# Kernel optimization log

Measured on AMD Instinct MI355X. Metric: run time of the kernel, lower is better.

## Reference

```python
import jax, jax.numpy as jnp
import numpy as np

B = 256   # batch == nodes (required by the module's mask broadcasting)
N = 256
F = 128   # in_features
H = 4     # num_heads
D = 8     # out_features (per-head dim)
E_RAND = 8192


def setup_inputs() -> dict:
    key = jax.random.key(0)
    ks = jax.random.split(key, 10)
    x = jax.random.normal(ks[0], (B, N, F), jnp.float32)
    # random edges + self-loops so every adjacency row is non-empty
    e = jax.random.randint(ks[1], (2, E_RAND), 0, B)
    diag = jnp.stack([jnp.arange(B), jnp.arange(B)])
    edge_index = jnp.concatenate([e, diag], axis=1)  # [2, 8448]
    s_in = 1.0 / np.sqrt(F)
    s_hd = 1.0 / np.sqrt(H * D)
    Wq = jax.random.normal(ks[2], (F, H * D), jnp.float32) * s_in
    Wk = jax.random.normal(ks[3], (F, H * D), jnp.float32) * s_in
    Wv = jax.random.normal(ks[4], (F, H * D), jnp.float32) * s_in
    Wo = jax.random.normal(ks[5], (H * D, D), jnp.float32) * s_hd
    bq = jax.random.normal(ks[6], (H * D,), jnp.float32) * s_in
    bk = jax.random.normal(ks[7], (H * D,), jnp.float32) * s_in
    bv = jax.random.normal(ks[8], (H * D,), jnp.float32) * s_in
    bo = jax.random.normal(ks[9], (D,), jnp.float32) * s_hd
    return dict(x=x, edge_index=edge_index, Wq=Wq, bq=bq, Wk=Wk, bk=bk,
                Wv=Wv, bv=bv, Wo=Wo, bo=bo)


def reference(x, edge_index, Wq, bq, Wk, bk, Wv, bv, Wo, bo):
    Bn, Nn, _ = x.shape
    q = (x @ Wq + bq).reshape(Bn, Nn, H, D)
    k = (x @ Wk + bk).reshape(Bn, Nn, H, D)
    v = (x @ Wv + bv).reshape(Bn, Nn, H, D)
    # [B, H, N, N]
    scores = jnp.einsum('bqhd,bkhd->bhqk', q, k) / jnp.sqrt(jnp.float32(D))
    # dense adjacency from sparse edge list, as in the original
    adj = jnp.zeros((Bn, Bn), x.dtype).at[edge_index[0], edge_index[1]].set(1.0)
    # mask [B,B] broadcasts over trailing (q,k) dims since N == B
    scores = jnp.where(adj == 0, -jnp.inf, scores)
    attn = jax.nn.softmax(scores, axis=-1)
    out = jnp.einsum('bhqk,bkhd->bqhd', attn, v).reshape(Bn, Nn, H * D)
    return out @ Wo + bo
```

## Files before the change

kernel.cpp:

```cpp
#include <hip/hip_runtime.h>

typedef unsigned int u32;
typedef __fp16 h2v __attribute__((ext_vector_type(2)));
typedef __fp16 h4 __attribute__((ext_vector_type(4)));
typedef float f32x16 __attribute__((ext_vector_type(16)));

#define NB 256
#define NNODE 256
#define FF 128
#define DD 8
#define HDIM 32

__device__ __forceinline__ float dot2(h2v a, h2v b, float c) {
  return __builtin_amdgcn_fdot2(a, b, c, false);
}
__device__ __forceinline__ h2v bch2(u32 u) { return __builtin_bit_cast(h2v, u); }
__device__ __forceinline__ h4 bch4(uint2 u) { return __builtin_bit_cast(h4, u); }
__device__ __forceinline__ u32 bcu(h2v v) { return __builtin_bit_cast(u32, v); }
__device__ __forceinline__ f32x16 fzero() {
  f32x16 z;
  #pragma unroll
  for (int r = 0; r < 16; ++r) z[r] = 0.f;
  return z;
}
__device__ __forceinline__ f32x16 mfma8(h4 a, h4 b, f32x16 c) {
  return __builtin_amdgcn_mfma_f32_32x32x8f16(a, b, c, 0, 0, 0);
}

__global__ __launch_bounds__(256) void prep_w_kernel(
    const float* __restrict__ Wq, const float* __restrict__ bq,
    const float* __restrict__ Wk, const float* __restrict__ bk,
    const float* __restrict__ Wv, const float* __restrict__ bv,
    const float* __restrict__ Wo,
    u32* __restrict__ mask, u32* __restrict__ WtH, float* __restrict__ bias,
    u32* __restrict__ woT2)
{
  int g = blockIdx.x * 256 + threadIdx.x;
  if (g < 96 * 64) {
    int c = g >> 6, f = (g & 63) * 2;
    const float* W = (c < 32) ? Wq : ((c < 64) ? Wk : Wv);
    int cc = c & 31;
    WtH[g] = bcu(__builtin_amdgcn_cvt_pkrtz(W[f*HDIM + cc], W[(f+1)*HDIM + cc]));
  }
  if (g < NNODE * 8) mask[g] = 0u;
  if (g < 96) {
    const float* bb = (g < 32) ? bq : ((g < 64) ? bk : bv);
    bias[g] = bb[g & 31];
  }
  if (g < 128) {
    int d = g >> 4, p = g & 15;
    woT2[g] = bcu(__builtin_amdgcn_cvt_pkrtz(Wo[(2*p)*DD + d], Wo[(2*p+1)*DD + d]));
  }
}

__global__ __launch_bounds__(256) void prep_e_kernel(
    const int* __restrict__ eidx, int E, u32* __restrict__ mask)
{
  int e = blockIdx.x * 256 + threadIdx.x;
  if (e < E) {
    int r = eidx[e], c = eidx[E + e];
    atomicOr(&mask[r*8 + (c >> 5)], 1u << (c & 31));
  }
}

__global__ __launch_bounds__(256, 2) void fused_kernel(
    const float* __restrict__ x, const u32* __restrict__ WtH,
    const float* __restrict__ bias, const u32* __restrict__ mask,
    const u32* __restrict__ woT2, const float* __restrict__ bo,
    float* __restrict__ out)
{
  __shared__ u32 wLds[96 * 66];
  __shared__ __fp16 kS[NNODE * 36];
  __shared__ __fp16 vt32[32 * 260];
  __shared__ __fp16 oS[128 * 36];
  __shared__ u32 woS[128];
  __shared__ float boS[8];

  int t = threadIdx.x, lane = t & 63, w = t >> 6;
  int l31 = lane & 31, hi = lane >> 5;
  int b = blockIdx.x >> 1, half = blockIdx.x & 1;

  for (int g = t; g < 96 * 64; g += 256)
    wLds[(g >> 6) * 66 + (g & 63)] = WtH[g];
  if (t < 128) woS[t] = woT2[t];
  if (t < 8) boS[t] = bo[t];

  f32x16 aq, ak0, av0, ak1, av1;
  #pragma unroll
  for (int r = 0; r < 16; ++r) aq[r] = bias[(r & 3) + 8*(r >> 2) + 4*hi];
  {
    float bk_ = bias[32 + l31], bv_ = bias[64 + l31];
    #pragma unroll
    for (int r = 0; r < 16; ++r) { ak0[r]=bk_; av0[r]=bv_; ak1[r]=bk_; av1[r]=bv_; }
  }

  int node = half*128 + w*32 + l31;
  uint4 m0 = *(const uint4*)(mask + node * 8);
  uint4 m1 = *(const uint4*)(mask + node * 8 + 4);
  u32 mw8[8] = { m0.x, m0.y, m0.z, m0.w, m1.x, m1.y, m1.z, m1.w };
  #pragma unroll
  for (int i = 0; i < 8; ++i) mw8[i] = hi ? (mw8[i] >> 4) : mw8[i];

  __syncthreads();

  const float* xr0 = x + ((size_t)b * NNODE + w*32 + l31) * FF + 4 * hi;
  const float* xr1 = xr0 + (size_t)128 * FF;
  #pragma unroll
  for (int ks = 0; ks < 16; ++ks) {
    float4 xf0 = *(const float4*)(xr0 + ks * 8);
    float4 xf1 = *(const float4*)(xr1 + ks * 8);
    h2v a0 = __builtin_amdgcn_cvt_pkrtz(xf0.x, xf0.y);
    h2v b0 = __builtin_amdgcn_cvt_pkrtz(xf0.z, xf0.w);
    h4 f0 = __builtin_shufflevector(a0, b0, 0, 1, 2, 3);
    h2v a1 = __builtin_amdgcn_cvt_pkrtz(xf1.x, xf1.y);
    h2v b1 = __builtin_amdgcn_cvt_pkrtz(xf1.z, xf1.w);
    h4 f1 = __builtin_shufflevector(a1, b1, 0, 1, 2, 3);
    h4 wk = bch4(*(const uint2*)&wLds[(32 + l31)*66 + ks*4 + 2*hi]);
    h4 wv = bch4(*(const uint2*)&wLds[(64 + l31)*66 + ks*4 + 2*hi]);
    h4 wq = bch4(*(const uint2*)&wLds[l31*66 + ks*4 + 2*hi]);
    ak0 = mfma8(f0, wk, ak0);
    ak1 = mfma8(f1, wk, ak1);
    av0 = mfma8(f0, wv, av0);
    av1 = mfma8(f1, wv, av1);
    aq  = mfma8(wq, half ? f1 : f0, aq);
  }
  #pragma unroll
  for (int r = 0; r < 16; ++r) {
    int rc = (r & 3) + 8*(r >> 2) + 4*hi;
    int n0 = w*32 + rc, n1 = n0 + 128;
    kS[n0 * 36 + l31] = (__fp16)ak0[r];
    kS[n1 * 36 + l31] = (__fp16)ak1[r];
    vt32[l31 * 260 + n0] = (__fp16)av0[r];
    vt32[l31 * 260 + n1] = (__fp16)av1[r];
  }
  h4 Qf[4];
  #pragma unroll
  for (int h = 0; h < 4; ++h) {
    h2v qa = __builtin_amdgcn_cvt_pkrtz(aq[4*h],     aq[4*h + 1]);
    h2v qb = __builtin_amdgcn_cvt_pkrtz(aq[4*h + 2], aq[4*h + 3]);
    Qf[h] = __builtin_shufflevector(qa, qb, 0, 1, 2, 3);
  }
  __syncthreads();

  const float sc2 = 0.51006977f;
  const h2v one2 = bch2(0x3C003C00u);
  f32x16 accO[4] = { fzero(), fzero(), fzero(), fzero() };
  float lp[4] = { 0.f, 0.f, 0.f, 0.f };
  #pragma unroll
  for (int kt = 0; kt < 8; ++kt) {
    u32 mwh = mw8[kt];
    float mbv[16];
    #pragma unroll
    for (int r = 0; r < 16; ++r) {
      int bp = (r & 3) + 8*(r >> 2);
      mbv[r] = ((mwh >> bp) & 1u) ? -8.0f : -1e30f;
    }
    u32 pw[4][8];
    #pragma unroll
    for (int h = 0; h < 4; ++h) {
      h4 Kf = bch4(*(const uint2*)&kS[(kt*32 + l31)*36 + 8*h + 4*hi]);
      f32x16 T = mfma8(Kf, Qf[h], fzero());
      #pragma unroll
      for (int j = 0; j < 8; ++j) {
        float p0 = __builtin_amdgcn_exp2f(__builtin_fmaf(T[2*j],   sc2, mbv[2*j]));
        float p1 = __builtin_amdgcn_exp2f(__builtin_fmaf(T[2*j+1], sc2, mbv[2*j+1]));
        pw[h][j] = bcu(__builtin_amdgcn_cvt_pkrtz(p0, p1));
        lp[h] = dot2(bch2(pw[h][j]), one2, lp[h]);
      }
    }
    __builtin_amdgcn_s_setprio(1);
    #pragma unroll
    for (int kk = 0; kk < 4; ++kk) {
      h4 va = bch4(*(const uint2*)&vt32[l31*260 + kt*32 + kk*8 + 4*hi]);
      #pragma unroll
      for (int h = 0; h < 4; ++h)
        accO[h] = mfma8(va, bch4(make_uint2(pw[h][2*kk], pw[h][2*kk+1])), accO[h]);
    }
    __builtin_amdgcn_s_setprio(0);
  }
  #pragma unroll
  for (int h = 0; h < 4; ++h) {
    float lq = lp[h] + __shfl_xor(lp[h], 32);
    float inv = 1.0f / lq;
    h2v o0 = __builtin_amdgcn_cvt_pkrtz(accO[h][4*h]*inv,   accO[h][4*h+1]*inv);
    h2v o1 = __builtin_amdgcn_cvt_pkrtz(accO[h][4*h+2]*inv, accO[h][4*h+3]*inv);
    *(uint2*)&oS[(w*32 + l31)*36 + 8*h + 4*hi] = make_uint2(bcu(o0), bcu(o1));
  }
  __syncthreads();

  int pr = t >> 1, d4 = (t & 1) * 4;
  float r4[4] = { boS[d4], boS[d4+1], boS[d4+2], boS[d4+3] };
  #pragma unroll
  for (int p = 0; p < 16; ++p) {
    h2v o2 = bch2(*(const u32*)&oS[pr*36 + 2*p]);
    #pragma unroll
    for (int d = 0; d < 4; ++d)
      r4[d] = dot2(o2, bch2(woS[(d4 + d)*16 + p]), r4[d]);
  }
  float4 o = { r4[0], r4[1], r4[2], r4[3] };
  *(float4*)(out + ((size_t)b * NNODE + half*128 + pr) * DD + d4) = o;
}

extern "C" void kernel_launch(void* const* d_in, const int* in_sizes, int n_in,
                              void* d_out, int out_size, void* d_ws, size_t ws_size,
                              hipStream_t stream)
{
  const float* x  = (const float*)d_in[0];
  const int*   ei = (const int*)d_in[1];
  const float* Wq = (const float*)d_in[2];
  const float* bq = (const float*)d_in[3];
  const float* Wk = (const float*)d_in[4];
  const float* bk = (const float*)d_in[5];
  const float* Wv = (const float*)d_in[6];
  const float* bv = (const float*)d_in[7];
  const float* Wo = (const float*)d_in[8];
  const float* bo = (const float*)d_in[9];
  int E = in_sizes[1] / 2;

  char* ws = (char*)d_ws;
  u32*   mask = (u32*)(ws + 0);
  u32*   WtH  = (u32*)(ws + 8192);
  float* bias = (float*)(ws + 32768);
  u32*   woT2 = (u32*)(ws + 33280);

  prep_w_kernel<<<24, 256, 0, stream>>>(Wq, bq, Wk, bk, Wv, bv, Wo,
                                        mask, WtH, bias, woT2);
  prep_e_kernel<<<(E + 255) / 256, 256, 0, stream>>>(ei, E, mask);
  fused_kernel<<<NB * 2, 256, 0, stream>>>(x, WtH, bias, mask, woT2, bo,
                                           (float*)d_out);
}
```

Measured before the change: 41.75 us.

## Merge prep kernels and fuse output projection into register epilogue

```diff
diff --git a/kernel.cpp b/kernel.cpp
--- a/kernel.cpp
+++ b/kernel.cpp
@@ -27,11 +27,11 @@
   return __builtin_amdgcn_mfma_f32_32x32x8f16(a, b, c, 0, 0, 0);
 }
 
-__global__ __launch_bounds__(256) void prep_w_kernel(
+__global__ __launch_bounds__(256) void prep_kernel(
     const float* __restrict__ Wq, const float* __restrict__ bq,
     const float* __restrict__ Wk, const float* __restrict__ bk,
     const float* __restrict__ Wv, const float* __restrict__ bv,
-    const float* __restrict__ Wo,
+    const float* __restrict__ Wo, const int* __restrict__ eidx, int E,
     u32* __restrict__ mask, u32* __restrict__ WtH, float* __restrict__ bias,
     u32* __restrict__ woT2)
 {
@@ -42,7 +42,6 @@
     int cc = c & 31;
     WtH[g] = bcu(__builtin_amdgcn_cvt_pkrtz(W[f*HDIM + cc], W[(f+1)*HDIM + cc]));
   }
-  if (g < NNODE * 8) mask[g] = 0u;
   if (g < 96) {
     const float* bb = (g < 32) ? bq : ((g < 64) ? bk : bv);
     bias[g] = bb[g & 31];
@@ -51,14 +50,8 @@
     int d = g >> 4, p = g & 15;
     woT2[g] = bcu(__builtin_amdgcn_cvt_pkrtz(Wo[(2*p)*DD + d], Wo[(2*p+1)*DD + d]));
   }
-}
-
-__global__ __launch_bounds__(256) void prep_e_kernel(
-    const int* __restrict__ eidx, int E, u32* __restrict__ mask)
-{
-  int e = blockIdx.x * 256 + threadIdx.x;
-  if (e < E) {
-    int r = eidx[e], c = eidx[E + e];
+  if (g < E) {
+    int r = eidx[g], c = eidx[E + g];
     atomicOr(&mask[r*8 + (c >> 5)], 1u << (c & 31));
   }
 }
@@ -72,7 +65,6 @@
   __shared__ u32 wLds[96 * 66];
   __shared__ __fp16 kS[NNODE * 36];
   __shared__ __fp16 vt32[32 * 260];
-  __shared__ __fp16 oS[128 * 36];
   __shared__ u32 woS[128];
   __shared__ float boS[8];
 
@@ -178,27 +170,28 @@
     }
     __builtin_amdgcn_s_setprio(0);
   }
+
+  float pa[8];
+  #pragma unroll
+  for (int dd = 0; dd < 8; ++dd) pa[dd] = 0.f;
   #pragma unroll
   for (int h = 0; h < 4; ++h) {
     float lq = lp[h] + __shfl_xor(lp[h], 32);
     float inv = 1.0f / lq;
-    h2v o0 = __builtin_amdgcn_cvt_pkrtz(accO[h][4*h]*inv,   accO[h][4*h+1]*inv);
-    h2v o1 = __builtin_amdgcn_cvt_pkrtz(accO[h][4*h+2]*inv, accO[h][4*h+3]*inv);
-    *(uint2*)&oS[(w*32 + l31)*36 + 8*h + 4*hi] = make_uint2(bcu(o0), bcu(o1));
-  }
-  __syncthreads();
-
-  int pr = t >> 1, d4 = (t & 1) * 4;
-  float r4[4] = { boS[d4], boS[d4+1], boS[d4+2], boS[d4+3] };
-  #pragma unroll
-  for (int p = 0; p < 16; ++p) {
-    h2v o2 = bch2(*(const u32*)&oS[pr*36 + 2*p]);
-    #pragma unroll
-    for (int d = 0; d < 4; ++d)
-      r4[d] = dot2(o2, bch2(woS[(d4 + d)*16 + p]), r4[d]);
-  }
-  float4 o = { r4[0], r4[1], r4[2], r4[3] };
-  *(float4*)(out + ((size_t)b * NNODE + half*128 + pr) * DD + d4) = o;
+    h2v o01 = __builtin_amdgcn_cvt_pkrtz(accO[h][4*h]*inv,   accO[h][4*h+1]*inv);
+    h2v o23 = __builtin_amdgcn_cvt_pkrtz(accO[h][4*h+2]*inv, accO[h][4*h+3]*inv);
+    #pragma unroll
+    for (int dd = 0; dd < 8; ++dd) {
+      pa[dd] = dot2(o01, bch2(woS[dd*16 + 4*h + 2*hi]),     pa[dd]);
+      pa[dd] = dot2(o23, bch2(woS[dd*16 + 4*h + 2*hi + 1]), pa[dd]);
+    }
+  }
+  #pragma unroll
+  for (int dd = 0; dd < 8; ++dd)
+    pa[dd] += __shfl_xor(pa[dd], 32);
+  float4 o4 = { pa[4*hi]   + boS[4*hi],   pa[4*hi+1] + boS[4*hi+1],
+                pa[4*hi+2] + boS[4*hi+2], pa[4*hi+3] + boS[4*hi+3] };
+  *(float4*)(out + ((size_t)b * NNODE + node) * DD + 4*hi) = o4;
 }
 
 extern "C" void kernel_launch(void* const* d_in, const int* in_sizes, int n_in,
@@ -223,9 +216,10 @@
   float* bias = (float*)(ws + 32768);
   u32*   woT2 = (u32*)(ws + 33280);
 
-  prep_w_kernel<<<24, 256, 0, stream>>>(Wq, bq, Wk, bk, Wv, bv, Wo,
-                                        mask, WtH, bias, woT2);
-  prep_e_kernel<<<(E + 255) / 256, 256, 0, stream>>>(ei, E, mask);
+  hipMemsetAsync(mask, 0, NNODE * 8 * sizeof(u32), stream);
+  int prep_work = (96*64 > E) ? 96*64 : E;
+  prep_kernel<<<(prep_work + 255)/256, 256, 0, stream>>>(
+      Wq, bq, Wk, bk, Wv, bv, Wo, ei, E, mask, WtH, bias, woT2);
   fused_kernel<<<NB * 2, 256, 0, stream>>>(x, WtH, bias, mask, woT2, bo,
                                            (float*)d_out);
 }
```

Measured after the change: 42.95 us. 1.03x slower.

## Merge prep kernels and split attention loop into two head-pair passes

Applied to the files above, without the earlier changes.

```diff
diff --git a/kernel.cpp b/kernel.cpp
--- a/kernel.cpp
+++ b/kernel.cpp
@@ -27,11 +27,11 @@
   return __builtin_amdgcn_mfma_f32_32x32x8f16(a, b, c, 0, 0, 0);
 }
 
-__global__ __launch_bounds__(256) void prep_w_kernel(
+__global__ __launch_bounds__(256) void prep_kernel(
     const float* __restrict__ Wq, const float* __restrict__ bq,
     const float* __restrict__ Wk, const float* __restrict__ bk,
     const float* __restrict__ Wv, const float* __restrict__ bv,
-    const float* __restrict__ Wo,
+    const float* __restrict__ Wo, const int* __restrict__ eidx, int E,
     u32* __restrict__ mask, u32* __restrict__ WtH, float* __restrict__ bias,
     u32* __restrict__ woT2)
 {
@@ -42,7 +42,6 @@
     int cc = c & 31;
     WtH[g] = bcu(__builtin_amdgcn_cvt_pkrtz(W[f*HDIM + cc], W[(f+1)*HDIM + cc]));
   }
-  if (g < NNODE * 8) mask[g] = 0u;
   if (g < 96) {
     const float* bb = (g < 32) ? bq : ((g < 64) ? bk : bv);
     bias[g] = bb[g & 31];
@@ -51,14 +50,8 @@
     int d = g >> 4, p = g & 15;
     woT2[g] = bcu(__builtin_amdgcn_cvt_pkrtz(Wo[(2*p)*DD + d], Wo[(2*p+1)*DD + d]));
   }
-}
-
-__global__ __launch_bounds__(256) void prep_e_kernel(
-    const int* __restrict__ eidx, int E, u32* __restrict__ mask)
-{
-  int e = blockIdx.x * 256 + threadIdx.x;
-  if (e < E) {
-    int r = eidx[e], c = eidx[E + e];
+  if (g < E) {
+    int r = eidx[g], c = eidx[E + g];
     atomicOr(&mask[r*8 + (c >> 5)], 1u << (c & 31));
   }
 }
@@ -144,47 +137,61 @@
 
   const float sc2 = 0.51006977f;
   const h2v one2 = bch2(0x3C003C00u);
-  f32x16 accO[4] = { fzero(), fzero(), fzero(), fzero() };
-  float lp[4] = { 0.f, 0.f, 0.f, 0.f };
-  #pragma unroll
-  for (int kt = 0; kt < 8; ++kt) {
-    u32 mwh = mw8[kt];
-    float mbv[16];
+  #pragma unroll
+  for (int hp = 0; hp < 2; ++hp) {
+    int h0 = 2*hp, h1 = 2*hp + 1;
+    f32x16 accO0 = fzero(), accO1 = fzero();
+    float lp0 = 0.f, lp1 = 0.f;
     #pragma unroll
-    for (int r = 0; r < 16; ++r) {
-      int bp = (r & 3) + 8*(r >> 2);
-      mbv[r] = ((mwh >> bp) & 1u) ? -8.0f : -1e30f;
+    for (int kt = 0; kt < 8; ++kt) {
+      u32 mwh = mw8[kt];
+      float mbv[16];
+      #pragma unroll
+      for (int r = 0; r < 16; ++r) {
+        int bp = (r & 3) + 8*(r >> 2);
+        mbv[r] = ((mwh >> bp) & 1u) ? -8.0f : -1e30f;
+      }
+      u32 pw0[8], pw1[8];
+      {
+        h4 Kf = bch4(*(const uint2*)&kS[(kt*32 + l31)*36 + 8*h0 + 4*hi]);
+        f32x16 T = mfma8(Kf, Qf[h0], fzero());
+        #pragma unroll
+        for (int j = 0; j < 8; ++j) {
+          float p0 = __builtin_amdgcn_exp2f(__builtin_fmaf(T[2*j],   sc2, mbv[2*j]));
+          float p1 = __builtin_amdgcn_exp2f(__builtin_fmaf(T[2*j+1], sc2, mbv[2*j+1]));
+          pw0[j] = bcu(__builtin_amdgcn_cvt_pkrtz(p0, p1));
+          lp0 = dot2(bch2(pw0[j]), one2, lp0);
+        }
+      }
+      {
+        h4 Kf = bch4(*(const uint2*)&kS[(kt*32 + l31)*36 + 8*h1 + 4*hi]);
+        f32x16 T = mfma8(Kf, Qf[h1], fzero());
+        #pragma unroll
+        for (int j = 0; j < 8; ++j) {
+          float p0 = __builtin_amdgcn_exp2f(__builtin_fmaf(T[2*j],   sc2, mbv[2*j]));
+          float p1 = __builtin_amdgcn_exp2f(__builtin_fmaf(T[2*j+1], sc2, mbv[2*j+1]));
+          pw1[j] = bcu(__builtin_amdgcn_cvt_pkrtz(p0, p1));
+          lp1 = dot2(bch2(pw1[j]), one2, lp1);
+        }
+      }
+      __builtin_amdgcn_s_setprio(1);
+      #pragma unroll
+      for (int kk = 0; kk < 4; ++kk) {
+        h4 va = bch4(*(const uint2*)&vt32[l31*260 + kt*32 + kk*8 + 4*hi]);
+        accO0 = mfma8(va, bch4(make_uint2(pw0[2*kk], pw0[2*kk+1])), accO0);
+        accO1 = mfma8(va, bch4(make_uint2(pw1[2*kk], pw1[2*kk+1])), accO1);
+      }
+      __builtin_amdgcn_s_setprio(0);
     }
-    u32 pw[4][8];
-    #pragma unroll
-    for (int h = 0; h < 4; ++h) {
-      h4 Kf = bch4(*(const uint2*)&kS[(kt*32 + l31)*36 + 8*h + 4*hi]);
-      f32x16 T = mfma8(Kf, Qf[h], fzero());
-      #pragma unroll
-      for (int j = 0; j < 8; ++j) {
-        float p0 = __builtin_amdgcn_exp2f(__builtin_fmaf(T[2*j],   sc2, mbv[2*j]));
-        float p1 = __builtin_amdgcn_exp2f(__builtin_fmaf(T[2*j+1], sc2, mbv[2*j+1]));
-        pw[h][j] = bcu(__builtin_amdgcn_cvt_pkrtz(p0, p1));
-        lp[h] = dot2(bch2(pw[h][j]), one2, lp[h]);
-      }
-    }
-    __builtin_amdgcn_s_setprio(1);
-    #pragma unroll
-    for (int kk = 0; kk < 4; ++kk) {
-      h4 va = bch4(*(const uint2*)&vt32[l31*260 + kt*32 + kk*8 + 4*hi]);
-      #pragma unroll
-      for (int h = 0; h < 4; ++h)
-        accO[h] = mfma8(va, bch4(make_uint2(pw[h][2*kk], pw[h][2*kk+1])), accO[h]);
-    }
-    __builtin_amdgcn_s_setprio(0);
-  }
-  #pragma unroll
-  for (int h = 0; h < 4; ++h) {
-    float lq = lp[h] + __shfl_xor(lp[h], 32);
-    float inv = 1.0f / lq;
-    h2v o0 = __builtin_amdgcn_cvt_pkrtz(accO[h][4*h]*inv,   accO[h][4*h+1]*inv);
-    h2v o1 = __builtin_amdgcn_cvt_pkrtz(accO[h][4*h+2]*inv, accO[h][4*h+3]*inv);
-    *(uint2*)&oS[(w*32 + l31)*36 + 8*h + 4*hi] = make_uint2(bcu(o0), bcu(o1));
+    float lq0 = lp0 + __shfl_xor(lp0, 32);
+    float lq1 = lp1 + __shfl_xor(lp1, 32);
+    float inv0 = 1.0f / lq0, inv1 = 1.0f / lq1;
+    h2v a0 = __builtin_amdgcn_cvt_pkrtz(accO0[4*h0]*inv0,   accO0[4*h0+1]*inv0);
+    h2v a1 = __builtin_amdgcn_cvt_pkrtz(accO0[4*h0+2]*inv0, accO0[4*h0+3]*inv0);
+    *(uint2*)&oS[(w*32 + l31)*36 + 8*h0 + 4*hi] = make_uint2(bcu(a0), bcu(a1));
+    h2v c0 = __builtin_amdgcn_cvt_pkrtz(accO1[4*h1]*inv1,   accO1[4*h1+1]*inv1);
+    h2v c1 = __builtin_amdgcn_cvt_pkrtz(accO1[4*h1+2]*inv1, accO1[4*h1+3]*inv1);
+    *(uint2*)&oS[(w*32 + l31)*36 + 8*h1 + 4*hi] = make_uint2(bcu(c0), bcu(c1));
   }
   __syncthreads();
 
@@ -223,9 +230,10 @@
   float* bias = (float*)(ws + 32768);
   u32*   woT2 = (u32*)(ws + 33280);
 
-  prep_w_kernel<<<24, 256, 0, stream>>>(Wq, bq, Wk, bk, Wv, bv, Wo,
-                                        mask, WtH, bias, woT2);
-  prep_e_kernel<<<(E + 255) / 256, 256, 0, stream>>>(ei, E, mask);
+  hipMemsetAsync(mask, 0, NNODE * 8 * sizeof(u32), stream);
+  int prep_work = (96*64 > E) ? 96*64 : E;
+  prep_kernel<<<(prep_work + 255)/256, 256, 0, stream>>>(
+      Wq, bq, Wk, bk, Wv, bv, Wo, ei, E, mask, WtH, bias, woT2);
   fused_kernel<<<NB * 2, 256, 0, stream>>>(x, WtH, bias, mask, woT2, bo,
                                            (float*)d_out);
 }
```

Result: slower. 42.78 us (+2.5%).
